# Kernel optimization log

Hardware: AMD Instinct MI355X
Metric: run time of the kernel (lower is better)

The kernel has to match this reference:

```python
import jax, jax.numpy as jnp
import numpy as np

N = 20000   # nodes
K = 32      # neighbors per node (kNN graph)
C = 128     # input feature dim
H = 256     # h_theta hidden/output dim
E = N * K   # edges


def setup_inputs() -> dict:
    key = jax.random.key(0)
    k1, k2, k3, k4 = jax.random.split(key, 4)
    node_features = jax.random.normal(k1, (N, C), dtype=jnp.float32)
    senders = jax.random.randint(k2, (E,), 0, N)              # neighbor node per edge
    receivers = jnp.repeat(jnp.arange(N), K)                  # center node per edge (k-NN: exactly K each)
    W1 = jax.random.normal(k3, (2 * C, H), dtype=jnp.float32) * (1.0 / np.sqrt(2 * C))
    b1 = jnp.zeros((H,), dtype=jnp.float32)
    W2 = jax.random.normal(k4, (H, H), dtype=jnp.float32) * (1.0 / np.sqrt(H))
    b2 = jnp.zeros((H,), dtype=jnp.float32)
    return {"node_features": node_features, "senders": senders, "receivers": receivers,
            "W1": W1, "b1": b1, "W2": W2, "b2": b2}


def reference(node_features, senders, receivers, W1, b1, W2, b2):
    # gather: x_v (center) and x_vp (neighbor) per edge -> [E, C]
    x_v = node_features[receivers]
    x_vp = node_features[senders]
    # edge feature: concat([x_v, x_vp - x_v]) -> [E, 2C]
    e = jnp.concatenate([x_v, x_vp - x_v], axis=-1)
    # h_theta MLP per edge -> [E, H]
    h = jnp.dot(jax.nn.relu(jnp.dot(e, W1) + b1), W2) + b2
    # max-reduce over each node's incident edges -> [N, H]
    return jax.ops.segment_max(h, receivers, num_segments=N)
```

## Files before the change

kernel.cpp:

```cpp
#include <hip/hip_runtime.h>
#include <hip/hip_bf16.h>

#define NN    20000
#define KNN   32
#define CIN   128
#define HD    256
#define EE    (NN * KNN)
#define MT    64
#define TPB   10
#define NBLK  (EE / (MT * TPB))

typedef __bf16 bf16x8_t __attribute__((ext_vector_type(8)));
typedef __bf16 bf16x4_t __attribute__((ext_vector_type(4)));
typedef float  f32x4_t  __attribute__((ext_vector_type(4)));

__device__ __forceinline__ void gload_lds16(const __bf16* g, __bf16* l) {
    __builtin_amdgcn_global_load_lds(
        (const __attribute__((address_space(1))) void*)g,
        (__attribute__((address_space(3))) void*)l, 16, 0, 0);
}

__global__ void ec_prep(const float* __restrict__ nf, const float* __restrict__ W1,
                        const float* __restrict__ W2, __bf16* __restrict__ nfb,
                        __bf16* __restrict__ w1g, __bf16* __restrict__ w2t) {
    int bid = blockIdx.x;
    if (bid < (NN * CIN) / 1024) {
        int i = (bid * 256 + threadIdx.x) * 4;
        float4 v = *(const float4*)(nf + i);
        bf16x4_t b = { (__bf16)v.x, (__bf16)v.y, (__bf16)v.z, (__bf16)v.w };
        *(bf16x4_t*)(nfb + i) = b;
    } else {
        int idx = (bid - (NN * CIN) / 1024) * 256 + threadIdx.x;
        int k = idx >> 8, n = idx & 255;
        float v = (k < CIN) ? (W1[k * 256 + n] - W1[(k + CIN) * 256 + n])
                            : W1[k * 256 + n];
        int kt = k >> 5, qr = (k >> 3) & 3, j = k & 7;
        w1g[(size_t)((kt * 4 + qr) * 256 + n) * 8 + j] = (__bf16)v;
        w2t[n * 256 + k] = (__bf16)W2[k * 256 + n];
    }
}

__global__ __launch_bounds__(512, 1) void ec_main(
    const __bf16* __restrict__ nfb,
    const int*   __restrict__ senders,
    const __bf16* __restrict__ w1g,
    const __bf16* __restrict__ w2t,
    const float* __restrict__ b1,
    const float* __restrict__ b2,
    float* __restrict__ out)
{
    __shared__ __attribute__((aligned(16))) __bf16 ldsW[32768];
    __shared__ __attribute__((aligned(16))) __bf16 ldsE[2][8192];
    __shared__ __attribute__((aligned(16))) __bf16 ldsH[16384];
    __shared__ __attribute__((aligned(16))) float  ldsY[20 * 256];

    const int tid  = threadIdx.x;
    const int lane = tid & 63;
    const int wave = tid >> 6;
    const int qrow = lane >> 4;
    const int lcol = lane & 15;
    const int blk  = blockIdx.x;
    const int fsl  = wave * 32;
    const int fs2  = (wave >> 1) * 64;
    const int eh   = wave & 1;
    const int p0 = wave * 2, p1 = wave * 2 + 1;
    const int c0 = p0 >> 2, q0 = p0 & 3;
    const int c1 = p1 >> 2, q1 = p1 & 3;

    int sidxAll[TPB];
#pragma unroll
    for (int tt = 0; tt < TPB; ++tt)
        sidxAll[tt] = senders[(blk * TPB + tt) * MT + lane];

    {
        const float4* src = (const float4*)(w1g + 32768);
        float4* dst = (float4*)ldsW;
#pragma unroll
        for (int i = 0; i < 8; ++i)
            dst[i * 512 + tid] = src[i * 512 + tid];
    }

    gload_lds16(nfb + (size_t)sidxAll[0] * CIN + c0 * 32 + q0 * 8, &ldsE[0][p0 * 512]);
    gload_lds16(nfb + (size_t)sidxAll[0] * CIN + c1 * 32 + q1 * 8, &ldsE[0][p1 * 512]);

    {
        f32x4_t ay[2][2];
#pragma unroll
        for (int mi = 0; mi < 2; ++mi)
#pragma unroll
            for (int ni = 0; ni < 2; ++ni)
                ay[mi][ni] = (f32x4_t){0.f, 0.f, 0.f, 0.f};
        bf16x8_t xv[2][4];
#pragma unroll
        for (int ni = 0; ni < 2; ++ni) {
            int ln = ni * 16 + lcol; if (ln > 19) ln = 19;
            const __bf16* row = nfb + (size_t)(blk * 20 + ln) * CIN;
#pragma unroll
            for (int c = 0; c < 4; ++c)
                xv[ni][c] = *(const bf16x8_t*)(row + c * 32 + qrow * 8);
        }
#pragma unroll
        for (int kt = 0; kt < 4; ++kt) {
            bf16x8_t wy[2];
#pragma unroll
            for (int mi = 0; mi < 2; ++mi)
                wy[mi] = *(const bf16x8_t*)(w1g +
                    (size_t)((kt * 4 + qrow) * 256 + fsl + mi * 16 + lcol) * 8);
#pragma unroll
            for (int mi = 0; mi < 2; ++mi)
#pragma unroll
                for (int ni = 0; ni < 2; ++ni)
                    ay[mi][ni] = __builtin_amdgcn_mfma_f32_16x16x32_bf16(
                        wy[mi], xv[ni][kt], ay[mi][ni], 0, 0, 0);
        }
#pragma unroll
        for (int mi = 0; mi < 2; ++mi)
#pragma unroll
            for (int ni = 0; ni < 2; ++ni) {
                int ln = ni * 16 + lcol;
                if (ln < 20)
                    *(f32x4_t*)(ldsY + ln * 256 + fsl + mi * 16 + qrow * 4) = ay[mi][ni];
            }
    }

    bf16x8_t w2f[8][4];
#pragma unroll
    for (int kt = 0; kt < 8; ++kt)
#pragma unroll
        for (int ni = 0; ni < 4; ++ni)
            w2f[kt][ni] = *(const bf16x8_t*)(w2t + (size_t)(fs2 + ni * 16 + lcol) * 256
                                                 + kt * 32 + qrow * 8);

    float4 bias1[2];
#pragma unroll
    for (int mi = 0; mi < 2; ++mi)
        bias1[mi] = *(const float4*)(b1 + fsl + mi * 16 + qrow * 4);
    float bias2[4];
#pragma unroll
    for (int ni = 0; ni < 4; ++ni)
        bias2[ni] = b2[fs2 + ni * 16 + lcol];

    __syncthreads();

#pragma unroll 1
    for (int t = 0; t < TPB; ++t) {
        const int node0 = (blk * TPB + t) * 2;
        const int cur = t & 1;

        if (t + 1 < TPB) {
            const __bf16* srow = nfb + (size_t)sidxAll[t + 1] * CIN;
            gload_lds16(srow + c0 * 32 + q0 * 8, &ldsE[1 - cur][p0 * 512]);
            gload_lds16(srow + c1 * 32 + q1 * 8, &ldsE[1 - cur][p1 * 512]);
        }

        f32x4_t acc[2][4];
#pragma unroll
        for (int mi = 0; mi < 2; ++mi)
#pragma unroll
            for (int ni = 0; ni < 4; ++ni)
                acc[mi][ni] = *(const f32x4_t*)(ldsY + (t * 2 + (ni >> 1)) * 256
                                                + fsl + mi * 16 + qrow * 4);
#pragma unroll
        for (int kt = 0; kt < 4; ++kt) {
            bf16x8_t wf[2], ef[4];
#pragma unroll
            for (int mi = 0; mi < 2; ++mi)
                wf[mi] = *(const bf16x8_t*)(ldsW +
                    (size_t)((kt * 4 + qrow) * 256 + fsl + mi * 16 + lcol) * 8);
#pragma unroll
            for (int ni = 0; ni < 4; ++ni)
                ef[ni] = *(const bf16x8_t*)(&ldsE[cur][0] +
                    (size_t)((kt * 4 + qrow) * 64 + ni * 16 + lcol) * 8);
#pragma unroll
            for (int mi = 0; mi < 2; ++mi)
#pragma unroll
                for (int ni = 0; ni < 4; ++ni)
                    acc[mi][ni] = __builtin_amdgcn_mfma_f32_16x16x32_bf16(
                        wf[mi], ef[ni], acc[mi][ni], 0, 0, 0);
        }

        __syncthreads();

#pragma unroll
        for (int mi = 0; mi < 2; ++mi) {
            const int f0  = fsl + mi * 16 + qrow * 4;
            const int ktp = f0 >> 5, qrp = (f0 >> 3) & 3, jh = f0 & 7;
            float4 bb = bias1[mi];
#pragma unroll
            for (int ni = 0; ni < 4; ++ni) {
                int edge = ni * 16 + lcol;
                float v0 = acc[mi][ni][0] + bb.x;
                float v1 = acc[mi][ni][1] + bb.y;
                float v2 = acc[mi][ni][2] + bb.z;
                float v3 = acc[mi][ni][3] + bb.w;
                bf16x4_t h = { (__bf16)fmaxf(v0, 0.f), (__bf16)fmaxf(v1, 0.f),
                               (__bf16)fmaxf(v2, 0.f), (__bf16)fmaxf(v3, 0.f) };
                *(bf16x4_t*)(ldsH + (size_t)((ktp * 4 + qrp) * 64 + edge) * 8 + jh) = h;
            }
        }
        __syncthreads();

        f32x4_t acc2[2][4];
#pragma unroll
        for (int mi = 0; mi < 2; ++mi)
#pragma unroll
            for (int ni = 0; ni < 4; ++ni)
                acc2[mi][ni] = (f32x4_t){0.f, 0.f, 0.f, 0.f};
#pragma unroll
        for (int kt = 0; kt < 8; ++kt) {
            bf16x8_t af[2];
#pragma unroll
            for (int mi = 0; mi < 2; ++mi)
                af[mi] = *(const bf16x8_t*)(ldsH +
                    (size_t)((kt * 4 + qrow) * 64 + eh * 32 + mi * 16 + lcol) * 8);
#pragma unroll
            for (int mi = 0; mi < 2; ++mi)
#pragma unroll
                for (int ni = 0; ni < 4; ++ni)
                    acc2[mi][ni] = __builtin_amdgcn_mfma_f32_16x16x32_bf16(
                        af[mi], w2f[kt][ni], acc2[mi][ni], 0, 0, 0);
        }

#pragma unroll
        for (int ni = 0; ni < 4; ++ni) {
            int col = fs2 + ni * 16 + lcol;
            float mx = -3.402823466e38f;
#pragma unroll
            for (int mi = 0; mi < 2; ++mi)
#pragma unroll
                for (int r = 0; r < 4; ++r)
                    mx = fmaxf(mx, acc2[mi][ni][r]);
            mx = fmaxf(mx, __shfl_xor(mx, 16, 64));
            mx = fmaxf(mx, __shfl_xor(mx, 32, 64));
            if (qrow == 0)
                out[(size_t)(node0 + eh) * HD + col] = mx + bias2[ni];
        }
    }
}

extern "C" void kernel_launch(void* const* d_in, const int* in_sizes, int n_in,
                              void* d_out, int out_size, void* d_ws, size_t ws_size,
                              hipStream_t stream) {
    const float* nf      = (const float*)d_in[0];
    const int*   senders = (const int*)d_in[1];
    const float* W1 = (const float*)d_in[3];
    const float* b1 = (const float*)d_in[4];
    const float* W2 = (const float*)d_in[5];
    const float* b2 = (const float*)d_in[6];

    __bf16* w1g = (__bf16*)d_ws;
    __bf16* w2t = w1g + 256 * 256;
    __bf16* nfb = w2t + 256 * 256;

    ec_prep<<<(NN * CIN) / 1024 + 256, 256, 0, stream>>>(nf, W1, W2, nfb, w1g, w2t);
    ec_main<<<NBLK, 512, 0, stream>>>(nfb, senders, w1g, w2t, b1, b2, (float*)d_out);
}
```

Before: 230.1 us.

## Shrink LDS: keep half of W1 in registers and store Y in bf16

Half of the neighbor-part W1 fragments now stay in registers instead of LDS, which halves the ldsW buffer. The per-node center projection Y is stored in LDS as bf16 with a padded stride instead of fp32. Sender indices are loaded per iteration instead of preloaded into a register array. The aim is to cut LDS footprint and LDS read traffic, and to ease register pressure from the index array. In exchange it adds bf16 rounding of Y, which affects accuracy, and raises register use for the W1 fragments.

```diff
diff --git a/kernel.cpp b/kernel.cpp
--- a/kernel.cpp
+++ b/kernel.cpp
@@ -9,6 +9,7 @@
 #define MT    64
 #define TPB   10
 #define NBLK  (EE / (MT * TPB))
+#define YSTR  264
 
 typedef __bf16 bf16x8_t __attribute__((ext_vector_type(8)));
 typedef __bf16 bf16x4_t __attribute__((ext_vector_type(4)));
@@ -49,10 +50,10 @@
     const float* __restrict__ b2,
     float* __restrict__ out)
 {
-    __shared__ __attribute__((aligned(16))) __bf16 ldsW[32768];
+    __shared__ __attribute__((aligned(16))) __bf16 ldsW[16384];
     __shared__ __attribute__((aligned(16))) __bf16 ldsE[2][8192];
     __shared__ __attribute__((aligned(16))) __bf16 ldsH[16384];
-    __shared__ __attribute__((aligned(16))) float  ldsY[20 * 256];
+    __shared__ __attribute__((aligned(16))) __bf16 ldsY[20 * YSTR];
 
     const int tid  = threadIdx.x;
     const int lane = tid & 63;
@@ -67,21 +68,19 @@
     const int c0 = p0 >> 2, q0 = p0 & 3;
     const int c1 = p1 >> 2, q1 = p1 & 3;
 
-    int sidxAll[TPB];
-#pragma unroll
-    for (int tt = 0; tt < TPB; ++tt)
-        sidxAll[tt] = senders[(blk * TPB + tt) * MT + lane];
-
     {
-        const float4* src = (const float4*)(w1g + 32768);
+        const float4* src = (const float4*)(w1g + 49152);
         float4* dst = (float4*)ldsW;
 #pragma unroll
-        for (int i = 0; i < 8; ++i)
+        for (int i = 0; i < 4; ++i)
             dst[i * 512 + tid] = src[i * 512 + tid];
     }
 
-    gload_lds16(nfb + (size_t)sidxAll[0] * CIN + c0 * 32 + q0 * 8, &ldsE[0][p0 * 512]);
-    gload_lds16(nfb + (size_t)sidxAll[0] * CIN + c1 * 32 + q1 * 8, &ldsE[0][p1 * 512]);
+    {
+        int s0 = senders[blk * TPB * MT + lane];
+        gload_lds16(nfb + (size_t)s0 * CIN + c0 * 32 + q0 * 8, &ldsE[0][p0 * 512]);
+        gload_lds16(nfb + (size_t)s0 * CIN + c1 * 32 + q1 * 8, &ldsE[0][p1 * 512]);
+    }
 
     {
         f32x4_t ay[2][2];
@@ -118,10 +117,21 @@
 #pragma unroll
             for (int ni = 0; ni < 2; ++ni) {
                 int ln = ni * 16 + lcol;
-                if (ln < 20)
-                    *(f32x4_t*)(ldsY + ln * 256 + fsl + mi * 16 + qrow * 4) = ay[mi][ni];
-            }
-    }
+                if (ln < 20) {
+                    bf16x4_t yb = { (__bf16)ay[mi][ni][0], (__bf16)ay[mi][ni][1],
+                                    (__bf16)ay[mi][ni][2], (__bf16)ay[mi][ni][3] };
+                    *(bf16x4_t*)(ldsY + ln * YSTR + fsl + mi * 16 + qrow * 4) = yb;
+                }
+            }
+    }
+
+    bf16x8_t w1s[2][2];
+#pragma unroll
+    for (int s = 0; s < 2; ++s)
+#pragma unroll
+        for (int mi = 0; mi < 2; ++mi)
+            w1s[s][mi] = *(const bf16x8_t*)(w1g +
+                (size_t)(((4 + s) * 4 + qrow) * 256 + fsl + mi * 16 + lcol) * 8);
 
     bf16x8_t w2f[8][4];
 #pragma unroll
@@ -148,7 +158,8 @@
         const int cur = t & 1;
 
         if (t + 1 < TPB) {
-            const __bf16* srow = nfb + (size_t)sidxAll[t + 1] * CIN;
+            int sN = senders[(blk * TPB + t + 1) * MT + lane];
+            const __bf16* srow = nfb + (size_t)sN * CIN;
             gload_lds16(srow + c0 * 32 + q0 * 8, &ldsE[1 - cur][p0 * 512]);
             gload_lds16(srow + c1 * 32 + q1 * 8, &ldsE[1 - cur][p1 * 512]);
         }
@@ -157,16 +168,21 @@
 #pragma unroll
         for (int mi = 0; mi < 2; ++mi)
 #pragma unroll
-            for (int ni = 0; ni < 4; ++ni)
-                acc[mi][ni] = *(const f32x4_t*)(ldsY + (t * 2 + (ni >> 1)) * 256
-                                                + fsl + mi * 16 + qrow * 4);
+            for (int ni = 0; ni < 4; ++ni) {
+                bf16x4_t yb = *(const bf16x4_t*)(ldsY + (t * 2 + (ni >> 1)) * YSTR
+                                                 + fsl + mi * 16 + qrow * 4);
+                acc[mi][ni] = (f32x4_t){ (float)yb[0], (float)yb[1],
+                                         (float)yb[2], (float)yb[3] };
+            }
 #pragma unroll
         for (int kt = 0; kt < 4; ++kt) {
             bf16x8_t wf[2], ef[4];
 #pragma unroll
-            for (int mi = 0; mi < 2; ++mi)
-                wf[mi] = *(const bf16x8_t*)(ldsW +
-                    (size_t)((kt * 4 + qrow) * 256 + fsl + mi * 16 + lcol) * 8);
+            for (int mi = 0; mi < 2; ++mi) {
+                if (kt < 2) wf[mi] = w1s[kt][mi];
+                else        wf[mi] = *(const bf16x8_t*)(ldsW +
+                    (size_t)(((kt - 2) * 4 + qrow) * 256 + fsl + mi * 16 + lcol) * 8);
+            }
 #pragma unroll
             for (int ni = 0; ni < 4; ++ni)
                 ef[ni] = *(const bf16x8_t*)(&ldsE[cur][0] +
```

Result: slower. 241.3 us (+4.9%).
